# Kernel tuning notes

Hardware: AMD Instinct MI355X
Metric: run time of the kernel (lower is better)

Reference implementation:

```python
import jax, jax.numpy as jnp
import numpy as np

B, S, D = 1, 4096, 1024
H, DH = 8, 128
SCALING = 256.0 ** -0.5
SOFTCAP = 50.0
WINDOW = 512
EPS = 1e-6
NEG = -1e30


def setup_inputs() -> dict:
    key = jax.random.key(0)
    ks = jax.random.split(key, 8)
    hidden_states = jax.random.normal(ks[0], (B, S, D), dtype=jnp.float32)
    # rope tables: plausible cos/sin in [-1,1]
    inv_freq = 1.0 / (10000.0 ** (jnp.arange(0, DH, 2, dtype=jnp.float32) / DH))
    t = jnp.arange(S, dtype=jnp.float32)
    freqs = jnp.outer(t, inv_freq)  # [S, DH/2]
    emb = jnp.concatenate([freqs, freqs], axis=-1)  # [S, DH]
    cos = jnp.cos(emb)[None]  # [1, S, DH]
    sin = jnp.sin(emb)[None]
    w = 0.02
    Wq = jax.random.normal(ks[1], (H * DH, D), dtype=jnp.float32) * w
    Wk = jax.random.normal(ks[2], (H * DH, D), dtype=jnp.float32) * w
    Wv = jax.random.normal(ks[3], (H * DH, D), dtype=jnp.float32) * w
    Wo = jax.random.normal(ks[4], (D, H * DH), dtype=jnp.float32) * w
    q_norm_w = jnp.zeros((DH,), dtype=jnp.float32)
    k_norm_w = jnp.zeros((DH,), dtype=jnp.float32)
    return {"hidden_states": hidden_states, "cos": cos, "sin": sin,
            "Wq": Wq, "Wk": Wk, "Wv": Wv, "Wo": Wo,
            "q_norm_w": q_norm_w, "k_norm_w": k_norm_w}


def _rms_norm(x, w):
    # Gemma3 RMSNorm: x * rsqrt(mean(x^2) + eps) * (1 + w)
    var = jnp.mean(jnp.square(x), axis=-1, keepdims=True)
    return x * jax.lax.rsqrt(var + EPS) * (1.0 + w)


def _rotate_half(x):
    x1, x2 = jnp.split(x, 2, axis=-1)
    return jnp.concatenate([-x2, x1], axis=-1)


def reference(hidden_states, cos, sin, Wq, Wk, Wv, Wo, q_norm_w, k_norm_w):
    b, s, _ = hidden_states.shape
    # QKV projections -> [B, H, S, DH]
    q = (hidden_states @ Wq.T).reshape(b, s, H, DH).transpose(0, 2, 1, 3)
    k = (hidden_states @ Wk.T).reshape(b, s, H, DH).transpose(0, 2, 1, 3)
    v = (hidden_states @ Wv.T).reshape(b, s, H, DH).transpose(0, 2, 1, 3)
    # per-head RMSNorm on q and k
    q = _rms_norm(q, q_norm_w)
    k = _rms_norm(k, k_norm_w)
    # RoPE (cos/sin broadcast over heads via unsqueeze(1))
    c = cos[:, None, :, :]
    si = sin[:, None, :, :]
    q = q * c + _rotate_half(q) * si
    k = k * c + _rotate_half(k) * si
    # scores with scaling and logit softcapping
    scores = jnp.einsum('bhqd,bhkd->bhqk', q, k) * SCALING
    scores = SOFTCAP * jnp.tanh(scores / SOFTCAP)
    # causal + sliding-window mask: attend to j with 0 <= i - j < WINDOW (plus j == i)
    i = jnp.arange(s)[:, None]
    j = jnp.arange(s)[None, :]
    mask = (j <= i) & (i - j < WINDOW)  # [S, S]
    scores = jnp.where(mask[None, None], scores, NEG)
    probs = jax.nn.softmax(scores, axis=-1)  # [B, H, S, S]
    attn = jnp.einsum('bhqk,bhkd->bhqd', probs, v)
    attn = attn.transpose(0, 2, 1, 3).reshape(b, s, H * DH)
    out = attn @ Wo.T
    return out, probs
```

## Files before the change

### kernel.cpp

```cpp
#include <hip/hip_runtime.h>

#define S_LEN 4096

typedef _Float16 f16;
typedef __bf16 bf16;
typedef __attribute__((ext_vector_type(4))) _Float16 f16x4;
typedef __attribute__((ext_vector_type(8))) _Float16 f16x8;
typedef __attribute__((ext_vector_type(8))) __bf16 bf16x8;
typedef __attribute__((ext_vector_type(4))) float f32x4;

__device__ __forceinline__ void async_cp16(void* lds, const void* g) {
  __builtin_amdgcn_global_load_lds((const __attribute__((address_space(1))) void*)g,
                                   (__attribute__((address_space(3))) void*)lds, 16, 0, 0);
}

__device__ __forceinline__ f32x4 mfma16(f16x8 a, f16x8 b, f32x4 c) {
  return __builtin_amdgcn_mfma_f32_16x16x32_f16(a, b, c, 0, 0, 0);
}

__global__ void detect_dtype(const unsigned short* __restrict__ x, int* __restrict__ flag) {
  const int t = threadIdx.x;
  int cnt = 0;
  for (int i = t; i < 16384; i += 256) {
    const int e = (x[i] >> 7) & 0xFF;
    cnt += (e >= 0x87);
  }
#pragma unroll
  for (int m = 1; m < 64; m <<= 1) cnt += __shfl_xor(cnt, m);
  __shared__ int red[4];
  if ((t & 63) == 0) red[t >> 6] = cnt;
  __syncthreads();
  if (t == 0) *flag = (red[0] + red[1] + red[2] + red[3] > 64) ? 1 : 0;
}

__device__ __forceinline__ void cvt8(const void* src, f16* dst, int i, int fp) {
  f16x8 o;
  if (fp) {
    const float* s = (const float*)src;
#pragma unroll
    for (int j = 0; j < 8; ++j) o[j] = (f16)s[i + j];
  } else {
    const bf16x8 v = *(const bf16x8*)((const bf16*)src + i);
#pragma unroll
    for (int j = 0; j < 8; ++j) o[j] = (f16)(float)v[j];
  }
  *(f16x8*)(dst + i) = o;
}

__global__ void cvt_all(const void* __restrict__ hs, const void* __restrict__ wq,
                        const void* __restrict__ wk, const void* __restrict__ wv,
                        const void* __restrict__ wo, const void* __restrict__ c,
                        const void* __restrict__ s, const void* __restrict__ qn,
                        const void* __restrict__ kn, f16* __restrict__ hsf,
                        f16* __restrict__ wqkv, f16* __restrict__ woh,
                        float* __restrict__ cd, float* __restrict__ sd,
                        float* __restrict__ qnd, float* __restrict__ knd,
                        const int* __restrict__ flagp) {
  const int fp = *flagp;
  const int b = blockIdx.x, tid = threadIdx.x;
  if (b < 2048) {
    cvt8(hs, hsf, (b * 256 + tid) * 8, fp);
  } else if (b < 4096) {
    const int bb = b - 2048;
    const int sub = bb >> 9;
    const int i = ((bb & 511) * 256 + tid) * 8;
    const void* src = (sub == 0) ? wq : (sub == 1) ? wk : (sub == 2) ? wv : wo;
    f16* dst = (sub < 3) ? (wqkv + (size_t)sub * 1048576) : woh;
    cvt8(src, dst, i, fp);
  } else if (b < 8192) {
    const int bb = b - 4096;
    const void* src = (bb < 2048) ? c : s;
    float* dst = (bb < 2048) ? cd : sd;
    const int i = (bb & 2047) * 256 + tid;
    dst[i] = fp ? ((const float*)src)[i] : (float)((const bf16*)src)[i];
  } else {
    if (tid < 128) qnd[tid] = fp ? ((const float*)qn)[tid] : (float)((const bf16*)qn)[tid];
    else knd[tid - 128] = fp ? ((const float*)kn)[tid - 128] : (float)((const bf16*)kn)[tid - 128];
  }
}

__device__ __forceinline__ void probs_zero_fill(void* dout, int fp, int fb, int nfb) {
  const int tid = threadIdx.x;
  if (fp) {
    float* pb = (float*)dout + 4194304;
    const int total = 8 * 4096 * 880;
    const f32x4 z = {};
    for (int u = fb * 256 + tid; u < total; u += nfb * 256) {
      const int rowid = (int)((unsigned)u / 880u);
      const int cu = u - rowid * 880;
      const int row = rowid & 4095;
      const int q0r = row & ~63;
      const int jc0 = (q0r >= 512) ? (((q0r - 511) >> 6) << 6) : 0;
      const int jc0c = jc0 >> 2;
      const int c4 = (cu < jc0c) ? (cu << 2) : (jc0 + 576 + ((cu - jc0c) << 2));
      __builtin_nontemporal_store(z, (f32x4*)&pb[((size_t)rowid << 12) + c4]);
    }
  } else {
    bf16* pb = (bf16*)dout + 4194304;
    const int total = 8 * 4096 * 440;
    const bf16x8 z = {};
    for (int u = fb * 256 + tid; u < total; u += nfb * 256) {
      const int rowid = (int)((unsigned)u / 440u);
      const int cu = u - rowid * 440;
      const int row = rowid & 4095;
      const int q0r = row & ~63;
      const int jc0 = (q0r >= 512) ? (((q0r - 511) >> 6) << 6) : 0;
      const int jc0c = jc0 >> 3;
      const int c8 = (cu < jc0c) ? (cu << 3) : (jc0 + 576 + ((cu - jc0c) << 3));
      __builtin_nontemporal_store(z, (bf16x8*)&pb[((size_t)rowid << 12) + c8]);
    }
  }
}

__launch_bounds__(256, 2)
__global__ void gemm_qkv(const f16* __restrict__ A, const f16* __restrict__ B,
                         const float* __restrict__ cosp, const float* __restrict__ sinp,
                         const float* __restrict__ qnw, const float* __restrict__ knw,
                         f16* __restrict__ qh, f16* __restrict__ kh, f16* __restrict__ vt) {
  __shared__ f16 smem[16384];
  f16* As = smem;
  f16* Bs = smem + 8192;
  const int tid = threadIdx.x;
  const int w = tid >> 6, l = tid & 63;
  const int n0 = blockIdx.x * 128, m0 = blockIdx.y * 128;
  const int wm = (w >> 1) * 64, wn = (w & 1) * 64;
  f32x4 acc[4][4] = {};
  for (int k0 = 0; k0 < 1024; k0 += 64) {
#pragma unroll
    for (int it = 0; it < 4; ++it) {
      const int c = it * 4 + w;
      const int row = c * 8 + (l >> 3);
      const int dq = (l & 7) ^ (row & 7);
      async_cp16(&As[c * 512], &A[(size_t)(m0 + row) * 1024 + k0 + dq * 8]);
      async_cp16(&Bs[c * 512], &B[(size_t)(n0 + row) * 1024 + k0 + dq * 8]);
    }
    __syncthreads();
#pragma unroll
    for (int ks = 0; ks < 2; ++ks) {
      f16x8 af[4], bfr[4];
#pragma unroll
      for (int i = 0; i < 4; ++i) {
        const int ra = wm + i * 16 + (l & 15);
        af[i] = *(const f16x8*)&As[ra * 64 + (((ks * 4 + (l >> 4)) ^ (ra & 7)) << 3)];
        const int rb = wn + i * 16 + (l & 15);
        bfr[i] = *(const f16x8*)&Bs[rb * 64 + (((ks * 4 + (l >> 4)) ^ (rb & 7)) << 3)];
      }
#pragma unroll
      for (int mi = 0; mi < 4; ++mi)
#pragma unroll
        for (int ni = 0; ni < 4; ++ni)
          acc[mi][ni] = mfma16(af[mi], bfr[ni], acc[mi][ni]);
    }
    __syncthreads();
  }
  const int part = blockIdx.x >> 3;
  const int h = blockIdx.x & 7;
#pragma unroll
  for (int mi = 0; mi < 4; ++mi)
#pragma unroll
    for (int ni = 0; ni < 4; ++ni) {
      const int col = wn + ni * 16 + (l & 15);
#pragma unroll
      for (int r = 0; r < 4; ++r) {
        const int row = wm + mi * 16 + ((l >> 4) << 2) + r;
        smem[row * 128 + (col ^ (((row >> 3) & 7) << 3))] = (f16)acc[mi][ni][r];
      }
    }
  __syncthreads();
  if (part == 2) {
#pragma unroll
    for (int it = 0; it < 8; ++it) {
      const int idx = it * 256 + tid;
      const int dh = idx >> 4;
      const int sl = (idx & 15) * 8;
      f16x8 o;
#pragma unroll
      for (int k = 0; k < 8; ++k)
        o[k] = smem[(sl + k) * 128 + (dh ^ ((((sl + k) >> 3) & 7) << 3))];
      *(f16x8*)&vt[((size_t)(h * 128 + dh)) * S_LEN + m0 + sl] = o;
    }
  } else {
    const float* nw = part ? knw : qnw;
    f16* outb = part ? kh : qh;
    const float nw0 = 1.f + nw[l], nw1 = 1.f + nw[l + 64];
#pragma unroll 4
    for (int rr = 0; rr < 32; ++rr) {
      const int row = w * 32 + rr;
      const int sg = m0 + row;
      const int cs = ((row >> 3) & 7) << 3;
      const float x0 = (float)smem[row * 128 + (l ^ cs)];
      const float x1 = (float)smem[row * 128 + ((l + 64) ^ cs)];
      float ssum = x0 * x0 + x1 * x1;
#pragma unroll
      for (int m = 1; m < 64; m <<= 1) ssum += __shfl_xor(ssum, m);
      const float rn = rsqrtf(ssum * (1.f / 128.f) + 1e-6f);
      const float g0 = rn * nw0, g1 = rn * nw1;
      const float c0 = cosp[sg * 128 + l], c1 = cosp[sg * 128 + l + 64];
      const float s0 = sinp[sg * 128 + l], s1 = sinp[sg * 128 + l + 64];
      f16* o = outb + ((size_t)h * S_LEN + sg) * 128;
      o[l] = (f16)(x0 * g0 * c0 - x1 * g1 * s0);
      o[l + 64] = (f16)(x1 * g1 * c1 + x0 * g0 * s1);
    }
  }
}

__launch_bounds__(256, 3)
__global__ void attn64(const f16* __restrict__ Qh, const f16* __restrict__ Kh,
                       const f16* __restrict__ Vt, f16* __restrict__ Pc,
                       f16* __restrict__ Oh, void* __restrict__ dout,
                       const int* __restrict__ flagp) {
  __shared__ f16 Qs[64 * 128];
  __shared__ f16 Ks[64 * 128];
  __shared__ f16 Vs[128 * 64];
  const int id = blockIdx.x;
  const int fp = *flagp;
  if (id >= 512) {
    probs_zero_fill(dout, fp, id - 512, gridDim.x - 512);
    return;
  }
  const int tid = threadIdx.x, w = tid >> 6, l = tid & 63;
  const int q0 = (id & 63) * 64, h = id >> 6;
  const int kt0 = (q0 >= 512) ? ((q0 - 511) >> 6) : 0;
  const int kt1 = (q0 + 64) >> 6;

#pragma unroll
  for (int it = 0; it < 4; ++it) {
    const int c = it * 4 + w;
    const int row = c * 4 + (l >> 4);
    const int dq = (l & 15) ^ (row & 15);
    async_cp16(&Qs[c * 512], &Qh[((size_t)h * S_LEN + q0 + row) * 128 + dq * 8]);
  }
  __syncthreads();
  f16x8 qfrag[4];
#pragma unroll
  for (int ks = 0; ks < 4; ++ks) {
    const int r = w * 16 + (l & 15);
    qfrag[ks] = *(const f16x8*)&Qs[r * 128 + (((ks * 4 + (l >> 4)) ^ (r & 15)) << 3)];
  }
  __syncthreads();

  f16* Ps = Qs + w * 1024;
  float* Ls = (float*)(Qs + 4096);
  float l_i[4] = {0.f, 0.f, 0.f, 0.f};
  f32x4 oacc[8] = {};

  for (int t = kt0; t < kt1; ++t) {
#pragma unroll
    for (int it = 0; it < 4; ++it) {
      const int c = it * 4 + w;
      { const int row = c * 4 + (l >> 4);
        const int dq = (l & 15) ^ (row & 15);
        async_cp16(&Ks[c * 512], &Kh[((size_t)h * S_LEN + t * 64 + row) * 128 + dq * 8]); }
      { const int row = c * 8 + (l >> 3);
        const int dq = (l & 7) ^ (row & 7);
        async_cp16(&Vs[c * 512], &Vt[((size_t)h * 128 + row) * S_LEN + t * 64 + dq * 8]); }
    }
    __syncthreads();
    f32x4 sacc[4] = {};
    __builtin_amdgcn_s_setprio(1);
#pragma unroll
    for (int ks = 0; ks < 4; ++ks) {
      f16x8 kfrag[4];
#pragma unroll
      for (int ni = 0; ni < 4; ++ni) {
        const int r = ni * 16 + (l & 15);
        kfrag[ni] = *(const f16x8*)&Ks[r * 128 + (((ks * 4 + (l >> 4)) ^ (r & 15)) << 3)];
      }
#pragma unroll
      for (int ni = 0; ni < 4; ++ni)
        sacc[ni] = mfma16(qfrag[ks], kfrag[ni], sacc[ni]);
    }
    __builtin_amdgcn_s_setprio(0);
#pragma unroll
    for (int reg = 0; reg < 4; ++reg) {
      const int pr = ((l >> 4) << 2) + reg;
      const int q = q0 + w * 16 + pr;
      float rs = 0.f;
#pragma unroll
      for (int ni = 0; ni < 4; ++ni) {
        const int col = t * 64 + ni * 16 + (l & 15);
        float s = sacc[ni][reg] * 0.0625f;
        const float z = __expf(s * 0.04f);
        s = 50.f * (1.f - 2.f / (z + 1.f));
        const bool valid = (col <= q) && (q - col < 512);
        const float p = valid ? __expf(s - 8.f) : 0.f;
        rs += p;
        const int pc = ni * 16 + (l & 15);
        Ps[pr * 64 + (((pc >> 3) ^ (pr & 7)) << 3) + (pc & 7)] = (f16)p;
      }
#pragma unroll
      for (int m = 1; m < 16; m <<= 1) rs += __shfl_xor(rs, m);
      l_i[reg] += rs;
    }
    __builtin_amdgcn_s_setprio(1);
#pragma unroll
    for (int ks = 0; ks < 2; ++ks) {
      const int rp = l & 15;
      const f16x8 pf = *(const f16x8*)&Ps[rp * 64 + (((ks * 4 + (l >> 4)) ^ (rp & 7)) << 3)];
      f16x8 vf[8];
#pragma unroll
      for (int ni = 0; ni < 8; ++ni) {
        const int r = ni * 16 + (l & 15);
        vf[ni] = *(const f16x8*)&Vs[r * 64 + (((ks * 4 + (l >> 4)) ^ (r & 7)) << 3)];
      }
#pragma unroll
      for (int ni = 0; ni < 8; ++ni)
        oacc[ni] = mfma16(pf, vf[ni], oacc[ni]);
    }
    __builtin_amdgcn_s_setprio(0);
    {
      const size_t rowbase = (size_t)h * 4096 + q0 + w * 16;
#pragma unroll
      for (int i = 0; i < 4; ++i) {
        const int pr = i * 4 + (l >> 4);
        const int pc = (l & 15) * 4;
        const f16x4 v = *(const f16x4*)&Ps[pr * 64 + (((pc >> 3) ^ (pr & 7)) << 3) + (pc & 7)];
        *(f16x4*)&Pc[(rowbase + pr) * 576 + (t - kt0) * 64 + pc] = v;
      }
    }
    __syncthreads();
  }

  float il[4];
#pragma unroll
  for (int r = 0; r < 4; ++r) il[r] = 1.f / l_i[r];
  if ((l & 15) == 0) {
#pragma unroll
    for (int r = 0; r < 4; ++r) Ls[w * 16 + ((l >> 4) << 2) + r] = il[r];
  }
#pragma unroll
  for (int ni = 0; ni < 8; ++ni) {
    const int row = q0 + w * 16 + ((l >> 4) << 2);
    const int col = h * 128 + ni * 16 + (l & 15);
#pragma unroll
    for (int r = 0; r < 4; ++r)
      Oh[(size_t)(row + r) * 1024 + col] = (f16)(oacc[ni][r] * il[r]);
  }
  __syncthreads();

  const int jc0 = kt0 * 64;
  const int W = (kt1 - kt0) * 64;
  if (fp) {
    float* pb = (float*)dout + 4194304;
    for (int u = tid; u < 64 * 144; u += 256) {
      const int row = (int)((unsigned)u / 144u);
      const int cu = u - row * 144;
      f32x4 v = {};
      if ((cu << 2) < W) {
        const float sc = Ls[row];
        const f16x4 pv = *(const f16x4*)&Pc[((size_t)(h << 12) + q0 + row) * 576 + (cu << 2)];
#pragma unroll
        for (int k = 0; k < 4; ++k) v[k] = (float)pv[k] * sc;
      }
      __builtin_nontemporal_store(
          v, (f32x4*)&pb[(((size_t)(h << 12) + q0 + row) << 12) + jc0 + (cu << 2)]);
    }
  } else {
    bf16* pb = (bf16*)dout + 4194304;
    for (int u = tid; u < 64 * 72; u += 256) {
      const int row = (int)((unsigned)u / 72u);
      const int cu = u - row * 72;
      bf16x8 v = {};
      if ((cu << 3) < W) {
        const float sc = Ls[row];
        const f16x8 pv = *(const f16x8*)&Pc[((size_t)(h << 12) + q0 + row) * 576 + (cu << 3)];
#pragma unroll
        for (int k = 0; k < 8; ++k) v[k] = (bf16)((float)pv[k] * sc);
      }
      __builtin_nontemporal_store(
          v, (bf16x8*)&pb[(((size_t)(h << 12) + q0 + row) << 12) + jc0 + (cu << 3)]);
    }
  }
}

__launch_bounds__(256, 2)
__global__ void gemmO(const f16* __restrict__ A, const f16* __restrict__ B,
                      void* __restrict__ dout, const int* __restrict__ flagp) {
  __shared__ f16 As[128 * 64];
  __shared__ f16 Bs[128 * 64];
  const int fp = *flagp;
  const int tid = threadIdx.x;
  const int w = tid >> 6, l = tid & 63;
  const int n0 = (blockIdx.x & 7) * 128, m0 = (blockIdx.x >> 3) * 128;
  const int wm = (w >> 1) * 64, wn = (w & 1) * 64;
  f32x4 acc[4][4] = {};
  for (int k0 = 0; k0 < 1024; k0 += 64) {
#pragma unroll
    for (int it = 0; it < 4; ++it) {
      const int c = it * 4 + w;
      const int row = c * 8 + (l >> 3);
      const int dq = (l & 7) ^ (row & 7);
      async_cp16(&As[c * 512], &A[(size_t)(m0 + row) * 1024 + k0 + dq * 8]);
      async_cp16(&Bs[c * 512], &B[(size_t)(n0 + row) * 1024 + k0 + dq * 8]);
    }
    __syncthreads();
#pragma unroll
    for (int ks = 0; ks < 2; ++ks) {
      f16x8 af[4], bfr[4];
#pragma unroll
      for (int i = 0; i < 4; ++i) {
        const int ra = wm + i * 16 + (l & 15);
        af[i] = *(const f16x8*)&As[ra * 64 + (((ks * 4 + (l >> 4)) ^ (ra & 7)) << 3)];
        const int rb = wn + i * 16 + (l & 15);
        bfr[i] = *(const f16x8*)&Bs[rb * 64 + (((ks * 4 + (l >> 4)) ^ (rb & 7)) << 3)];
      }
#pragma unroll
      for (int mi = 0; mi < 4; ++mi)
#pragma unroll
        for (int ni = 0; ni < 4; ++ni)
          acc[mi][ni] = mfma16(af[mi], bfr[ni], acc[mi][ni]);
    }
    __syncthreads();
  }
#pragma unroll
  for (int mi = 0; mi < 4; ++mi)
#pragma unroll
    for (int ni = 0; ni < 4; ++ni) {
      const int col = n0 + wn + ni * 16 + (l & 15);
      const int row = m0 + wm + mi * 16 + ((l >> 4) << 2);
#pragma unroll
      for (int r = 0; r < 4; ++r) {
        const size_t off = (size_t)(row + r) * 1024 + col;
        if (fp) ((float*)dout)[off] = acc[mi][ni][r];
        else    ((bf16*)dout)[off] = (bf16)acc[mi][ni][r];
      }
    }
}

extern "C" void kernel_launch(void* const* d_in, const int* in_sizes, int n_in,
                              void* d_out, int out_size, void* d_ws, size_t ws_size,
                              hipStream_t stream) {
  (void)in_sizes; (void)n_in; (void)out_size; (void)ws_size;
  char* ws = (char*)d_ws;
  f16*   Pc    = (f16*)(ws);
  f16*   qh    = (f16*)(ws + (36u << 20));
  f16*   kh    = (f16*)(ws + (44u << 20));
  f16*   vt    = (f16*)(ws + (52u << 20));
  f16*   attnh = (f16*)(ws + (60u << 20));
  f16*   woh   = (f16*)(ws + (68u << 20));
  f16*   hsf   = (f16*)(ws + (70u << 20));
  f16*   wqkv  = (f16*)(ws + (78u << 20));
  float* cosf  = (float*)(ws + (84u << 20));
  float* sinf  = (float*)(ws + (86u << 20));
  float* qnwf  = (float*)(ws + (88u << 20));
  float* knwf  = (float*)(ws + (88u << 20) + 512);
  int*   flag  = (int*)(ws + (88u << 20) + 1024);

  detect_dtype<<<1, 256, 0, stream>>>((const unsigned short*)d_in[0], flag);
  cvt_all<<<8193, 256, 0, stream>>>(d_in[0], d_in[3], d_in[4], d_in[5], d_in[6],
                                    d_in[1], d_in[2], d_in[7], d_in[8],
                                    hsf, wqkv, woh, cosf, sinf, qnwf, knwf, flag);
  gemm_qkv<<<dim3(24, 32), 256, 0, stream>>>(hsf, wqkv, cosf, sinf, qnwf, knwf, qh, kh, vt);
  attn64<<<2048, 256, 0, stream>>>(qh, kh, vt, Pc, attnh, d_out, flag);
  gemmO<<<256, 256, 0, stream>>>(attnh, woh, d_out, flag);
}
```

Before: 663.8 us.

## Enlarge attention query tile from 64 to 128 rows per block

The attention kernel now processes 128 query rows per block, with each wave handling 32 rows, so each loaded K/V tile is reused across twice as many queries. The probability staging buffer widens to 640 columns, the zero-fill region shrinks to match the wider dense band, and the workspace offsets shift. The trade-offs are more registers, a larger LDS footprint (occupancy hint drops to 2), more wasted masked columns per tile, and fewer attention blocks with fewer zero-fill blocks.

```diff
diff --git a/kernel.cpp b/kernel.cpp
--- a/kernel.cpp
+++ b/kernel.cpp
@@ -83,30 +83,30 @@
   const int tid = threadIdx.x;
   if (fp) {
     float* pb = (float*)dout + 4194304;
-    const int total = 8 * 4096 * 880;
+    const int total = 8 * 4096 * 864;
     const f32x4 z = {};
     for (int u = fb * 256 + tid; u < total; u += nfb * 256) {
-      const int rowid = (int)((unsigned)u / 880u);
-      const int cu = u - rowid * 880;
+      const int rowid = (int)((unsigned)u / 864u);
+      const int cu = u - rowid * 864;
       const int row = rowid & 4095;
-      const int q0r = row & ~63;
+      const int q0r = row & ~127;
       const int jc0 = (q0r >= 512) ? (((q0r - 511) >> 6) << 6) : 0;
       const int jc0c = jc0 >> 2;
-      const int c4 = (cu < jc0c) ? (cu << 2) : (jc0 + 576 + ((cu - jc0c) << 2));
+      const int c4 = (cu < jc0c) ? (cu << 2) : (jc0 + 640 + ((cu - jc0c) << 2));
       __builtin_nontemporal_store(z, (f32x4*)&pb[((size_t)rowid << 12) + c4]);
     }
   } else {
     bf16* pb = (bf16*)dout + 4194304;
-    const int total = 8 * 4096 * 440;
+    const int total = 8 * 4096 * 432;
     const bf16x8 z = {};
     for (int u = fb * 256 + tid; u < total; u += nfb * 256) {
-      const int rowid = (int)((unsigned)u / 440u);
-      const int cu = u - rowid * 440;
+      const int rowid = (int)((unsigned)u / 432u);
+      const int cu = u - rowid * 432;
       const int row = rowid & 4095;
-      const int q0r = row & ~63;
+      const int q0r = row & ~127;
       const int jc0 = (q0r >= 512) ? (((q0r - 511) >> 6) << 6) : 0;
       const int jc0c = jc0 >> 3;
-      const int c8 = (cu < jc0c) ? (cu << 3) : (jc0 + 576 + ((cu - jc0c) << 3));
+      const int c8 = (cu < jc0c) ? (cu << 3) : (jc0 + 640 + ((cu - jc0c) << 3));
       __builtin_nontemporal_store(z, (bf16x8*)&pb[((size_t)rowid << 12) + c8]);
     }
   }
@@ -204,45 +204,47 @@
   }
 }
 
-__launch_bounds__(256, 3)
-__global__ void attn64(const f16* __restrict__ Qh, const f16* __restrict__ Kh,
-                       const f16* __restrict__ Vt, f16* __restrict__ Pc,
-                       f16* __restrict__ Oh, void* __restrict__ dout,
-                       const int* __restrict__ flagp) {
-  __shared__ f16 Qs[64 * 128];
+__launch_bounds__(256, 2)
+__global__ void attn128(const f16* __restrict__ Qh, const f16* __restrict__ Kh,
+                        const f16* __restrict__ Vt, f16* __restrict__ Pc,
+                        f16* __restrict__ Oh, void* __restrict__ dout,
+                        const int* __restrict__ flagp) {
+  __shared__ f16 Qs[128 * 128];
   __shared__ f16 Ks[64 * 128];
   __shared__ f16 Vs[128 * 64];
   const int id = blockIdx.x;
   const int fp = *flagp;
-  if (id >= 512) {
-    probs_zero_fill(dout, fp, id - 512, gridDim.x - 512);
+  if (id >= 256) {
+    probs_zero_fill(dout, fp, id - 256, gridDim.x - 256);
     return;
   }
   const int tid = threadIdx.x, w = tid >> 6, l = tid & 63;
-  const int q0 = (id & 63) * 64, h = id >> 6;
+  const int q0 = (id & 31) * 128, h = id >> 5;
   const int kt0 = (q0 >= 512) ? ((q0 - 511) >> 6) : 0;
-  const int kt1 = (q0 + 64) >> 6;
-
-#pragma unroll
-  for (int it = 0; it < 4; ++it) {
+  const int kt1 = (q0 + 128) >> 6;
+
+#pragma unroll
+  for (int it = 0; it < 8; ++it) {
     const int c = it * 4 + w;
     const int row = c * 4 + (l >> 4);
     const int dq = (l & 15) ^ (row & 15);
     async_cp16(&Qs[c * 512], &Qh[((size_t)h * S_LEN + q0 + row) * 128 + dq * 8]);
   }
   __syncthreads();
-  f16x8 qfrag[4];
-#pragma unroll
-  for (int ks = 0; ks < 4; ++ks) {
-    const int r = w * 16 + (l & 15);
-    qfrag[ks] = *(const f16x8*)&Qs[r * 128 + (((ks * 4 + (l >> 4)) ^ (r & 15)) << 3)];
-  }
+  f16x8 qfrag[2][4];
+#pragma unroll
+  for (int mi = 0; mi < 2; ++mi)
+#pragma unroll
+    for (int ks = 0; ks < 4; ++ks) {
+      const int r = w * 32 + mi * 16 + (l & 15);
+      qfrag[mi][ks] = *(const f16x8*)&Qs[r * 128 + (((ks * 4 + (l >> 4)) ^ (r & 15)) << 3)];
+    }
   __syncthreads();
 
-  f16* Ps = Qs + w * 1024;
-  float* Ls = (float*)(Qs + 4096);
-  float l_i[4] = {0.f, 0.f, 0.f, 0.f};
-  f32x4 oacc[8] = {};
+  f16* Ps = Qs + w * 2048;
+  float* Ls = (float*)(Qs + 8192);
+  float l_i[8] = {};
+  f32x4 oacc[2][8] = {};
 
   for (int t = kt0; t < kt1; ++t) {
 #pragma unroll
@@ -256,7 +258,7 @@
         async_cp16(&Vs[c * 512], &Vt[((size_t)h * 128 + row) * S_LEN + t * 64 + dq * 8]); }
     }
     __syncthreads();
-    f32x4 sacc[4] = {};
+    f32x4 sacc[2][4] = {};
     __builtin_amdgcn_s_setprio(1);
 #pragma unroll
     for (int ks = 0; ks < 4; ++ks) {
@@ -267,88 +269,103 @@
         kfrag[ni] = *(const f16x8*)&Ks[r * 128 + (((ks * 4 + (l >> 4)) ^ (r & 15)) << 3)];
       }
 #pragma unroll
-      for (int ni = 0; ni < 4; ++ni)
-        sacc[ni] = mfma16(qfrag[ks], kfrag[ni], sacc[ni]);
+      for (int mi = 0; mi < 2; ++mi)
+#pragma unroll
+        for (int ni = 0; ni < 4; ++ni)
+          sacc[mi][ni] = mfma16(qfrag[mi][ks], kfrag[ni], sacc[mi][ni]);
     }
     __builtin_amdgcn_s_setprio(0);
 #pragma unroll
-    for (int reg = 0; reg < 4; ++reg) {
-      const int pr = ((l >> 4) << 2) + reg;
-      const int q = q0 + w * 16 + pr;
-      float rs = 0.f;
-#pragma unroll
-      for (int ni = 0; ni < 4; ++ni) {
-        const int col = t * 64 + ni * 16 + (l & 15);
-        float s = sacc[ni][reg] * 0.0625f;
-        const float z = __expf(s * 0.04f);
-        s = 50.f * (1.f - 2.f / (z + 1.f));
-        const bool valid = (col <= q) && (q - col < 512);
-        const float p = valid ? __expf(s - 8.f) : 0.f;
-        rs += p;
-        const int pc = ni * 16 + (l & 15);
-        Ps[pr * 64 + (((pc >> 3) ^ (pr & 7)) << 3) + (pc & 7)] = (f16)p;
-      }
-#pragma unroll
-      for (int m = 1; m < 16; m <<= 1) rs += __shfl_xor(rs, m);
-      l_i[reg] += rs;
-    }
+    for (int mi = 0; mi < 2; ++mi)
+#pragma unroll
+      for (int reg = 0; reg < 4; ++reg) {
+        const int i = mi * 4 + reg;
+        const int pr = mi * 16 + ((l >> 4) << 2) + reg;
+        const int q = q0 + w * 32 + pr;
+        float rs = 0.f;
+#pragma unroll
+        for (int ni = 0; ni < 4; ++ni) {
+          const int col = t * 64 + ni * 16 + (l & 15);
+          float s = sacc[mi][ni][reg] * 0.0625f;
+          const float z = __expf(s * 0.04f);
+          s = 50.f * (1.f - 2.f / (z + 1.f));
+          const bool valid = (col <= q) && (q - col < 512);
+          const float p = valid ? __expf(s - 8.f) : 0.f;
+          rs += p;
+          const int pc = ni * 16 + (l & 15);
+          Ps[pr * 64 + (((pc >> 3) ^ (pr & 7)) << 3) + (pc & 7)] = (f16)p;
+        }
+#pragma unroll
+        for (int m = 1; m < 16; m <<= 1) rs += __shfl_xor(rs, m);
+        l_i[i] += rs;
+      }
     __builtin_amdgcn_s_setprio(1);
 #pragma unroll
     for (int ks = 0; ks < 2; ++ks) {
-      const int rp = l & 15;
-      const f16x8 pf = *(const f16x8*)&Ps[rp * 64 + (((ks * 4 + (l >> 4)) ^ (rp & 7)) << 3)];
-      f16x8 vf[8];
+      f16x8 pf[2], vf[8];
+#pragma unroll
+      for (int mi = 0; mi < 2; ++mi) {
+        const int r = mi * 16 + (l & 15);
+        pf[mi] = *(const f16x8*)&Ps[r * 64 + (((ks * 4 + (l >> 4)) ^ (r & 7)) << 3)];
+      }
 #pragma unroll
       for (int ni = 0; ni < 8; ++ni) {
         const int r = ni * 16 + (l & 15);
         vf[ni] = *(const f16x8*)&Vs[r * 64 + (((ks * 4 + (l >> 4)) ^ (r & 7)) << 3)];
       }
 #pragma unroll
-      for (int ni = 0; ni < 8; ++ni)
-        oacc[ni] = mfma16(pf, vf[ni], oacc[ni]);
+      for (int mi = 0; mi < 2; ++mi)
+#pragma unroll
+        for (int ni = 0; ni < 8; ++ni)
+          oacc[mi][ni] = mfma16(pf[mi], vf[ni], oacc[mi][ni]);
     }
     __builtin_amdgcn_s_setprio(0);
     {
-      const size_t rowbase = (size_t)h * 4096 + q0 + w * 16;
-#pragma unroll
-      for (int i = 0; i < 4; ++i) {
+      const size_t rowbase = (size_t)h * 4096 + q0 + w * 32;
+#pragma unroll
+      for (int i = 0; i < 8; ++i) {
         const int pr = i * 4 + (l >> 4);
         const int pc = (l & 15) * 4;
         const f16x4 v = *(const f16x4*)&Ps[pr * 64 + (((pc >> 3) ^ (pr & 7)) << 3) + (pc & 7)];
-        *(f16x4*)&Pc[(rowbase + pr) * 576 + (t - kt0) * 64 + pc] = v;
-      }
-    }
-    __syncthreads();
-  }
-
-  float il[4];
-#pragma unroll
-  for (int r = 0; r < 4; ++r) il[r] = 1.f / l_i[r];
+        *(f16x4*)&Pc[(rowbase + pr) * 640 + (t - kt0) * 64 + pc] = v;
+      }
+    }
+    __syncthreads();
+  }
+
+  float il[8];
+#pragma unroll
+  for (int r = 0; r < 8; ++r) il[r] = 1.f / l_i[r];
   if ((l & 15) == 0) {
 #pragma unroll
-    for (int r = 0; r < 4; ++r) Ls[w * 16 + ((l >> 4) << 2) + r] = il[r];
-  }
-#pragma unroll
-  for (int ni = 0; ni < 8; ++ni) {
-    const int row = q0 + w * 16 + ((l >> 4) << 2);
-    const int col = h * 128 + ni * 16 + (l & 15);
-#pragma unroll
-    for (int r = 0; r < 4; ++r)
-      Oh[(size_t)(row + r) * 1024 + col] = (f16)(oacc[ni][r] * il[r]);
-  }
+    for (int mi = 0; mi < 2; ++mi)
+#pragma unroll
+      for (int r = 0; r < 4; ++r)
+        Ls[w * 32 + mi * 16 + ((l >> 4) << 2) + r] = il[mi * 4 + r];
+  }
+#pragma unroll
+  for (int mi = 0; mi < 2; ++mi)
+#pragma unroll
+    for (int ni = 0; ni < 8; ++ni) {
+      const int row = q0 + w * 32 + mi * 16 + ((l >> 4) << 2);
+      const int col = h * 128 + ni * 16 + (l & 15);
+#pragma unroll
+      for (int r = 0; r < 4; ++r)
+        Oh[(size_t)(row + r) * 1024 + col] = (f16)(oacc[mi][ni][r] * il[mi * 4 + r]);
+    }
   __syncthreads();
 
   const int jc0 = kt0 * 64;
   const int W = (kt1 - kt0) * 64;
   if (fp) {
     float* pb = (float*)dout + 4194304;
-    for (int u = tid; u < 64 * 144; u += 256) {
-      const int row = (int)((unsigned)u / 144u);
-      const int cu = u - row * 144;
+    for (int u = tid; u < 128 * 160; u += 256) {
+      const int row = (int)((unsigned)u / 160u);
+      const int cu = u - row * 160;
       f32x4 v = {};
       if ((cu << 2) < W) {
         const float sc = Ls[row];
-        const f16x4 pv = *(const f16x4*)&Pc[((size_t)(h << 12) + q0 + row) * 576 + (cu << 2)];
+        const f16x4 pv = *(const f16x4*)&Pc[((size_t)(h << 12) + q0 + row) * 640 + (cu << 2)];
 #pragma unroll
         for (int k = 0; k < 4; ++k) v[k] = (float)pv[k] * sc;
       }
@@ -357,13 +374,13 @@
     }
   } else {
     bf16* pb = (bf16*)dout + 4194304;
-    for (int u = tid; u < 64 * 72; u += 256) {
-      const int row = (int)((unsigned)u / 72u);
-      const int cu = u - row * 72;
+    for (int u = tid; u < 128 * 80; u += 256) {
+      const int row = (int)((unsigned)u / 80u);
+      const int cu = u - row * 80;
       bf16x8 v = {};
       if ((cu << 3) < W) {
         const float sc = Ls[row];
-        const f16x8 pv = *(const f16x8*)&Pc[((size_t)(h << 12) + q0 + row) * 576 + (cu << 3)];
+        const f16x8 pv = *(const f16x8*)&Pc[((size_t)(h << 12) + q0 + row) * 640 + (cu << 3)];
 #pragma unroll
         for (int k = 0; k < 8; ++k) v[k] = (bf16)((float)pv[k] * sc);
       }
@@ -433,24 +450,24 @@
   (void)in_sizes; (void)n_in; (void)out_size; (void)ws_size;
   char* ws = (char*)d_ws;
   f16*   Pc    = (f16*)(ws);
-  f16*   qh    = (f16*)(ws + (36u << 20));
-  f16*   kh    = (f16*)(ws + (44u << 20));
-  f16*   vt    = (f16*)(ws + (52u << 20));
-  f16*   attnh = (f16*)(ws + (60u << 20));
-  f16*   woh   = (f16*)(ws + (68u << 20));
-  f16*   hsf   = (f16*)(ws + (70u << 20));
-  f16*   wqkv  = (f16*)(ws + (78u << 20));
-  float* cosf  = (float*)(ws + (84u << 20));
-  float* sinf  = (float*)(ws + (86u << 20));
-  float* qnwf  = (float*)(ws + (88u << 20));
-  float* knwf  = (float*)(ws + (88u << 20) + 512);
-  int*   flag  = (int*)(ws + (88u << 20) + 1024);
+  f16*   qh    = (f16*)(ws + (40u << 20));
+  f16*   kh    = (f16*)(ws + (48u << 20));
+  f16*   vt    = (f16*)(ws + (56u << 20));
+  f16*   attnh = (f16*)(ws + (64u << 20));
+  f16*   woh   = (f16*)(ws + (72u << 20));
+  f16*   hsf   = (f16*)(ws + (74u << 20));
+  f16*   wqkv  = (f16*)(ws + (82u << 20));
+  float* cosf  = (float*)(ws + (88u << 20));
+  float* sinf  = (float*)(ws + (90u << 20));
+  float* qnwf  = (float*)(ws + (92u << 20));
+  float* knwf  = (float*)(ws + (92u << 20) + 512);
+  int*   flag  = (int*)(ws + (92u << 20) + 1024);
 
   detect_dtype<<<1, 256, 0, stream>>>((const unsigned short*)d_in[0], flag);
   cvt_all<<<8193, 256, 0, stream>>>(d_in[0], d_in[3], d_in[4], d_in[5], d_in[6],
                                     d_in[1], d_in[2], d_in[7], d_in[8],
                                     hsf, wqkv, woh, cosf, sinf, qnwf, knwf, flag);
   gemm_qkv<<<dim3(24, 32), 256, 0, stream>>>(hsf, wqkv, cosf, sinf, qnwf, knwf, qh, kh, vt);
-  attn64<<<2048, 256, 0, stream>>>(qh, kh, vt, Pc, attnh, d_out, flag);
+  attn128<<<1024, 256, 0, stream>>>(qh, kh, vt, Pc, attnh, d_out, flag);
   gemmO<<<256, 256, 0, stream>>>(attnh, woh, d_out, flag);
 }
```

Result: slower. 719.8 us (+8.4%).
